# Performance work log

Measured on AMD Instinct MI355X. Metric: run time of the kernel, lower is better.

The kernel has to match this reference:

```python
import jax, jax.numpy as jnp
import numpy as np

NUM_HEADING_BIN = 12
NUM_SIZE_CLUSTER = 8
DELTA_NORM_W = 0.01
CENTER_W = 0.5
B, N = 4096, 2048


def huber(err, delta=1.0):
    a = jnp.abs(err)
    q = jnp.minimum(a, delta)
    return jnp.mean(0.5 * q * q + delta * (a - q))


def box3d_corners(centers, headings, sizes):
    # centers (B,3), headings (B,), sizes (B,3) -> (B,8,3)
    l, w, h = sizes[:, 0:1], sizes[:, 1:2], sizes[:, 2:3]
    sx = jnp.asarray([1, 1, -1, -1, 1, 1, -1, -1], dtype=sizes.dtype)
    sy = jnp.asarray([1, -1, -1, 1, 1, -1, -1, 1], dtype=sizes.dtype)
    sz = jnp.asarray([1, 1, 1, 1, -1, -1, -1, -1], dtype=sizes.dtype)
    corners = jnp.stack([0.5 * l * sx, 0.5 * w * sy, 0.5 * h * sz], axis=1)  # (B,3,8)
    c, s = jnp.cos(headings), jnp.sin(headings)
    z, o = jnp.zeros_like(c), jnp.ones_like(c)
    R = jnp.stack([jnp.stack([c, -s, z], -1),
                   jnp.stack([s, c, z], -1),
                   jnp.stack([z, z, o], -1)], axis=1)  # (B,3,3)
    out = jnp.einsum('bij,bjk->bik', R, corners) + centers[:, :, None]
    return jnp.transpose(out, (0, 2, 1))  # (B,8,3)


def setup_inputs() -> dict:
    key = jax.random.key(0)
    ks = jax.random.split(key, 9)
    return {
        'mask_xyz_mean': jax.random.normal(ks[0], (B, 3), jnp.float32),
        'point_cloud': jax.random.normal(ks[1], (B, 3, N), jnp.float32),
        'x_delta': jax.random.normal(ks[2], (B, 3, N), jnp.float32),
        'center_label': jax.random.normal(ks[3], (B, 3), jnp.float32),
        'size_residual_label': jax.random.normal(ks[4], (B, 3), jnp.float32),
        'heading_residual_label': jax.random.normal(ks[5], (B,), jnp.float32),
        'mean_sizes': jax.random.uniform(ks[6], (NUM_SIZE_CLUSTER, 3), jnp.float32, 0.5, 2.5),
        'size_class_label': jax.random.randint(ks[7], (B,), 0, NUM_SIZE_CLUSTER, jnp.int32),
        'heading_class_label': jax.random.randint(ks[8], (B,), 0, NUM_HEADING_BIN, jnp.int32),
    }


def reference(mask_xyz_mean, point_cloud, x_delta, center_label,
              size_residual_label, heading_residual_label, mean_sizes,
              size_class_label, heading_class_label):
    eps = 0.0  # faithful: original has no eps
    # center loss
    center_dist = jnp.linalg.norm(mask_xyz_mean - center_label, axis=1)
    center_loss = CENTER_W * huber(center_dist)

    # label assembly (onehot-sum == gather)
    size_label = mean_sizes[size_class_label] + size_residual_label  # (B,3)
    bin_centers = jnp.arange(0, np.pi, np.pi / NUM_HEADING_BIN, dtype=jnp.float32)
    heading_label = heading_residual_label + bin_centers[heading_class_label]  # (B,)

    corners_3d_gt = box3d_corners(center_label, heading_label, size_label)
    corners_2d_gt = corners_3d_gt[:, 4:8, :2]  # (B,4,2)

    v = center_label[:, :2]  # (B,2)
    p_dir = jnp.stack([-v[:, 1], v[:, 0]], axis=1)
    p_dir = p_dir / jnp.linalg.norm(p_dir, axis=1, keepdims=True)  # (B,2)

    pp_label = jnp.einsum('bkc,bc->bk', corners_2d_gt, p_dir)  # (B,4)
    py_max, py_min = jnp.max(pp_label, axis=1), jnp.min(pp_label, axis=1)
    std_y_label = (py_max - py_min) / 4
    mean_y_label = (py_max + py_min) / 2

    v_norm = jnp.linalg.norm(v, axis=1, keepdims=True)  # (B,1)
    proj_label = jnp.einsum('bkc,bc->bk', corners_2d_gt, v) / v_norm  # (B,4)
    p_max, p_min = jnp.max(proj_label, axis=1), jnp.min(proj_label, axis=1)
    std_label = (p_max - p_min) / 4
    mean_label = (p_max + p_min) / 2

    pc_xy = jnp.transpose(point_cloud, (0, 2, 1))[:, :, :2]  # (B,N,2)

    pp_pc = jnp.einsum('bnc,bc->bn', pc_xy, p_dir)  # (B,N)
    std_y_pc = jnp.std(pp_pc, axis=1, ddof=1)
    mean_y_pc = jnp.mean(pp_pc, axis=1)
    y_std_loss = huber(jnp.abs(std_y_label - std_y_pc))
    y_mean_loss = huber(jnp.abs(mean_y_label - mean_y_pc))

    proj_pc = jnp.einsum('bnc,bc->bn', pc_xy, v) / v_norm  # (B,N)
    std_pc = jnp.std(proj_pc, axis=1, ddof=1)
    mean_pc = jnp.mean(proj_pc, axis=1)
    x_std_loss = huber(jnp.abs(std_label - std_pc))
    x_mean_loss = huber(jnp.abs(mean_label - mean_pc))

    delta_norm = jnp.sqrt(jnp.sum(x_delta * x_delta, axis=(1, 2)))
    delta_norm_loss = DELTA_NORM_W * huber(delta_norm)

    total = center_loss + x_std_loss + x_mean_loss + delta_norm_loss + y_mean_loss + y_std_loss
    return 0.4 * total
```

## Files before the change

### kernel.cpp

```cpp
#include <hip/hip_runtime.h>
#include <math.h>

#define B_SZ 4096
#define N_PTS 2048
#define BLOCK 256

__global__ void zero_out_kernel(float* out) { out[0] = 0.0f; }

__device__ __forceinline__ float huber1(float a) {
    float q = fminf(a, 1.0f);
    return 0.5f * q * q + (a - q);
}

__global__ __launch_bounds__(BLOCK) void loss_kernel(
    const float* __restrict__ mask_xyz_mean,
    const float* __restrict__ point_cloud,
    const float* __restrict__ x_delta,
    const float* __restrict__ center_label,
    const float* __restrict__ size_residual,
    const float* __restrict__ heading_residual,
    const float* __restrict__ mean_sizes,
    const int*   __restrict__ size_class,
    const int*   __restrict__ heading_class,
    float* __restrict__ out)
{
    const int b   = blockIdx.x;
    const int tid = threadIdx.x;

    const float cx = center_label[b * 3 + 0];
    const float cy = center_label[b * 3 + 1];

    const float vnorm2 = cx * cx + cy * cy;
    const float vnorm  = sqrtf(vnorm2);
    const float pdx = -cy / vnorm;
    const float pdy =  cx / vnorm;

    const size_t base = (size_t)b * 3 * N_PTS;
    const float4* px4 = (const float4*)(point_cloud + base);
    const float4* py4 = (const float4*)(point_cloud + base + N_PTS);
    const float4* pd4 = (const float4*)(x_delta + base);

    float s_pp = 0.f, s_pp2 = 0.f, s_t = 0.f, s_t2 = 0.f, s_d2 = 0.f;

    #pragma unroll
    for (int k = 0; k < N_PTS / 4 / BLOCK; ++k) {
        const int i = tid + k * BLOCK;
        const float4 x4 = px4[i];
        const float4 y4 = py4[i];
        {
            float pp = x4.x * pdx + y4.x * pdy;
            float t  = x4.x * cx  + y4.x * cy;
            s_pp += pp; s_pp2 += pp * pp; s_t += t; s_t2 += t * t;
        }
        {
            float pp = x4.y * pdx + y4.y * pdy;
            float t  = x4.y * cx  + y4.y * cy;
            s_pp += pp; s_pp2 += pp * pp; s_t += t; s_t2 += t * t;
        }
        {
            float pp = x4.z * pdx + y4.z * pdy;
            float t  = x4.z * cx  + y4.z * cy;
            s_pp += pp; s_pp2 += pp * pp; s_t += t; s_t2 += t * t;
        }
        {
            float pp = x4.w * pdx + y4.w * pdy;
            float t  = x4.w * cx  + y4.w * cy;
            s_pp += pp; s_pp2 += pp * pp; s_t += t; s_t2 += t * t;
        }
    }

    #pragma unroll
    for (int k = 0; k < 3 * N_PTS / 4 / BLOCK; ++k) {
        const int i = tid + k * BLOCK;
        const float4 d = pd4[i];
        s_d2 += d.x * d.x + d.y * d.y + d.z * d.z + d.w * d.w;
    }

    #pragma unroll
    for (int off = 32; off > 0; off >>= 1) {
        s_pp  += __shfl_down(s_pp,  off, 64);
        s_pp2 += __shfl_down(s_pp2, off, 64);
        s_t   += __shfl_down(s_t,   off, 64);
        s_t2  += __shfl_down(s_t2,  off, 64);
        s_d2  += __shfl_down(s_d2,  off, 64);
    }

    __shared__ float red[BLOCK / 64][5];
    const int wave = tid >> 6;
    const int lane = tid & 63;
    if (lane == 0) {
        red[wave][0] = s_pp;  red[wave][1] = s_pp2;
        red[wave][2] = s_t;   red[wave][3] = s_t2;
        red[wave][4] = s_d2;
    }
    __syncthreads();

    if (tid == 0) {
        #pragma unroll
        for (int w = 1; w < BLOCK / 64; ++w) {
            s_pp  += red[w][0];
            s_pp2 += red[w][1];
            s_t   += red[w][2];
            s_t2  += red[w][3];
            s_d2  += red[w][4];
        }

        const float mx = mask_xyz_mean[b * 3 + 0];
        const float my = mask_xyz_mean[b * 3 + 1];
        const float mz = mask_xyz_mean[b * 3 + 2];
        const float cz = center_label[b * 3 + 2];
        const float dxc = mx - cx, dyc = my - cy, dzc = mz - cz;
        const float center_dist = sqrtf(dxc * dxc + dyc * dyc + dzc * dzc);

        const int sc = size_class[b];
        const float l  = mean_sizes[sc * 3 + 0] + size_residual[b * 3 + 0];
        const float w_ = mean_sizes[sc * 3 + 1] + size_residual[b * 3 + 1];

        const float theta = heading_residual[b] +
                            (float)heading_class[b] * (float)(M_PI / 12.0);
        const float c = cosf(theta);
        const float s = sinf(theta);
        const float hl = 0.5f * l, hw = 0.5f * w_;

        float X[4], Y[4];
        X[0] =  c * hl - s * hw + cx;  Y[0] =  s * hl + c * hw + cy;
        X[1] =  c * hl + s * hw + cx;  Y[1] =  s * hl - c * hw + cy;
        X[2] = -c * hl + s * hw + cx;  Y[2] = -s * hl - c * hw + cy;
        X[3] = -c * hl - s * hw + cx;  Y[3] = -s * hl + c * hw + cy;

        float ppmax = -INFINITY, ppmin = INFINITY;
        float pmax  = -INFINITY, pmin  = INFINITY;
        #pragma unroll
        for (int k = 0; k < 4; ++k) {
            const float pp = X[k] * pdx + Y[k] * pdy;
            const float pj = (X[k] * cx + Y[k] * cy) / vnorm;
            ppmax = fmaxf(ppmax, pp); ppmin = fminf(ppmin, pp);
            pmax  = fmaxf(pmax,  pj); pmin  = fminf(pmin,  pj);
        }
        const float std_y_label  = (ppmax - ppmin) * 0.25f;
        const float mean_y_label = (ppmax + ppmin) * 0.5f;
        const float std_label    = (pmax - pmin) * 0.25f;
        const float mean_label   = (pmax + pmin) * 0.5f;

        const float invN = 1.0f / (float)N_PTS;
        const float invNm1 = 1.0f / (float)(N_PTS - 1);

        const float mean_y_pc = s_pp * invN;
        const float var_y = (s_pp2 - s_pp * s_pp * invN) * invNm1;
        const float std_y_pc = sqrtf(fmaxf(var_y, 0.0f));

        const float mean_pc = (s_t * invN) / vnorm;
        const float var_x = ((s_t2 - s_t * s_t * invN) * invNm1) / vnorm2;
        const float std_pc = sqrtf(fmaxf(var_x, 0.0f));

        const float delta_norm = sqrtf(s_d2);

        const float total =
              0.5f  * huber1(center_dist)
            +         huber1(fabsf(std_label  - std_pc))
            +         huber1(fabsf(mean_label - mean_pc))
            + 0.01f * huber1(delta_norm)
            +         huber1(fabsf(mean_y_label - mean_y_pc))
            +         huber1(fabsf(std_y_label  - std_y_pc));

        atomicAdd(out, total * (0.4f / (float)B_SZ));
    }
}

extern "C" void kernel_launch(void* const* d_in, const int* in_sizes, int n_in,
                              void* d_out, int out_size, void* d_ws, size_t ws_size,
                              hipStream_t stream) {
    const float* mask_xyz_mean    = (const float*)d_in[0];
    const float* point_cloud      = (const float*)d_in[1];
    const float* x_delta          = (const float*)d_in[2];
    const float* center_label     = (const float*)d_in[3];
    const float* size_residual    = (const float*)d_in[4];
    const float* heading_residual = (const float*)d_in[5];
    const float* mean_sizes       = (const float*)d_in[6];
    const int*   size_class       = (const int*)d_in[7];
    const int*   heading_class    = (const int*)d_in[8];
    float* out = (float*)d_out;

    zero_out_kernel<<<1, 1, 0, stream>>>(out);
    loss_kernel<<<B_SZ, BLOCK, 0, stream>>>(
        mask_xyz_mean, point_cloud, x_delta, center_label, size_residual,
        heading_residual, mean_sizes, size_class, heading_class, out);
}
```

Before: 232.2 us.

## Assign one wavefront per batch row and drop block-level reduction

Each 64-lane wavefront now handles a whole batch element instead of a 256-thread block, so the grid shrinks by four and the shared-memory reduction and __syncthreads go away. Each lane does more loads per row (unroll 8 on the delta loop), which raises per-thread memory-level parallelism. The zeroing kernel is replaced by hipMemsetAsync. There are four times as many atomicAdds per block, but the same total count.

New measurement: 246.5 us. 6.2% more time.

```diff
diff --git a/kernel.cpp b/kernel.cpp
--- a/kernel.cpp
+++ b/kernel.cpp
@@ -4,8 +4,8 @@
 #define B_SZ 4096
 #define N_PTS 2048
 #define BLOCK 256
-
-__global__ void zero_out_kernel(float* out) { out[0] = 0.0f; }
+#define WPB (BLOCK / 64)
+#define GRID (B_SZ / WPB)
 
 __device__ __forceinline__ float huber1(float a) {
     float q = fminf(a, 1.0f);
@@ -24,8 +24,9 @@
     const int*   __restrict__ heading_class,
     float* __restrict__ out)
 {
-    const int b   = blockIdx.x;
-    const int tid = threadIdx.x;
+    const int wave = threadIdx.x >> 6;
+    const int lane = threadIdx.x & 63;
+    const int b    = blockIdx.x * WPB + wave;
 
     const float cx = center_label[b * 3 + 0];
     const float cy = center_label[b * 3 + 1];
@@ -43,8 +44,8 @@
     float s_pp = 0.f, s_pp2 = 0.f, s_t = 0.f, s_t2 = 0.f, s_d2 = 0.f;
 
     #pragma unroll
-    for (int k = 0; k < N_PTS / 4 / BLOCK; ++k) {
-        const int i = tid + k * BLOCK;
+    for (int k = 0; k < N_PTS / 4 / 64; ++k) {
+        const int i = lane + k * 64;
         const float4 x4 = px4[i];
         const float4 y4 = py4[i];
         {
@@ -69,9 +70,9 @@
         }
     }
 
-    #pragma unroll
-    for (int k = 0; k < 3 * N_PTS / 4 / BLOCK; ++k) {
-        const int i = tid + k * BLOCK;
+    #pragma unroll 8
+    for (int k = 0; k < 3 * N_PTS / 4 / 64; ++k) {
+        const int i = lane + k * 64;
         const float4 d = pd4[i];
         s_d2 += d.x * d.x + d.y * d.y + d.z * d.z + d.w * d.w;
     }
@@ -85,26 +86,7 @@
         s_d2  += __shfl_down(s_d2,  off, 64);
     }
 
-    __shared__ float red[BLOCK / 64][5];
-    const int wave = tid >> 6;
-    const int lane = tid & 63;
     if (lane == 0) {
-        red[wave][0] = s_pp;  red[wave][1] = s_pp2;
-        red[wave][2] = s_t;   red[wave][3] = s_t2;
-        red[wave][4] = s_d2;
-    }
-    __syncthreads();
-
-    if (tid == 0) {
-        #pragma unroll
-        for (int w = 1; w < BLOCK / 64; ++w) {
-            s_pp  += red[w][0];
-            s_pp2 += red[w][1];
-            s_t   += red[w][2];
-            s_t2  += red[w][3];
-            s_d2  += red[w][4];
-        }
-
         const float mx = mask_xyz_mean[b * 3 + 0];
         const float my = mask_xyz_mean[b * 3 + 1];
         const float mz = mask_xyz_mean[b * 3 + 2];
@@ -142,7 +124,7 @@
         const float std_label    = (pmax - pmin) * 0.25f;
         const float mean_label   = (pmax + pmin) * 0.5f;
 
-        const float invN = 1.0f / (float)N_PTS;
+        const float invN   = 1.0f / (float)N_PTS;
         const float invNm1 = 1.0f / (float)(N_PTS - 1);
 
         const float mean_y_pc = s_pp * invN;
@@ -181,8 +163,8 @@
     const int*   heading_class    = (const int*)d_in[8];
     float* out = (float*)d_out;
 
-    zero_out_kernel<<<1, 1, 0, stream>>>(out);
-    loss_kernel<<<B_SZ, BLOCK, 0, stream>>>(
+    hipMemsetAsync(out, 0, sizeof(float), stream);
+    loss_kernel<<<GRID, BLOCK, 0, stream>>>(
         mask_xyz_mean, point_cloud, x_delta, center_label, size_residual,
         heading_residual, mean_sizes, size_class, heading_class, out);
 }
```
